# Optimization experiments

Measured on AMD Instinct MI355X. Metric: run time of the kernel, lower is better.

Reference implementation:

```python
import jax, jax.numpy as jnp
import numpy as np

T, B, H = 2048, 8, 1024


def setup_inputs() -> dict:
    key = jax.random.key(0)
    ks = jax.random.split(key, 4)
    scale = 1.0 / np.sqrt(H)
    x = jax.random.normal(ks[0], (T, B, H), dtype=jnp.float32)
    W_q = jax.random.normal(ks[1], (H, H), dtype=jnp.float32) * scale
    b_q = jnp.zeros((H,), dtype=jnp.float32)
    beta_raw = jax.random.normal(ks[2], (H,), dtype=jnp.float32)
    W_fc = jax.random.normal(ks[3], (H, H), dtype=jnp.float32) * scale
    b_fc = jnp.zeros((H,), dtype=jnp.float32)
    return {"x": x, "W_q": W_q, "b_q": b_q, "beta_raw": beta_raw,
            "W_fc": W_fc, "b_fc": b_fc}


def reference(x, W_q, b_q, beta_raw, W_fc, b_fc):
    # Per-neuron learned leak in (0,1)
    beta = jax.nn.sigmoid(beta_raw)  # (H,)
    # Input (q) projection: (T,B,H) @ (H,H)^T
    q = jnp.einsum('tbh,oh->tbo', x, W_q) + b_q  # (T,B,H)
    # Leaky integration m_t = beta * m_{t-1} + q_t as an associative scan over T
    a = jnp.broadcast_to(beta, q.shape)  # (T,B,H)

    def combine(c1, c2):
        a1, m1 = c1
        a2, m2 = c2
        return (a1 * a2, a2 * m1 + m2)

    _, m = jax.lax.associative_scan(combine, (a, q), axis=0)  # (T,B,H)
    # Linear + ReLU
    h = jnp.einsum('tbh,oh->tbo', m, W_fc) + b_fc
    return jax.nn.relu(h)
```

## Files before the change

kernel.cpp:

```cpp
#include <hip/hip_runtime.h>
#include <stdint.h>

typedef unsigned short u16;
typedef __bf16 bf16x8 __attribute__((ext_vector_type(8)));
typedef float f32x4 __attribute__((ext_vector_type(4)));

__device__ __forceinline__ u16 f2bf(float f) {
  union { float f; uint32_t u; } x; x.f = f;
  uint32_t u = x.u;
  u += 0x7fffu + ((u >> 16) & 1u);
  return (u16)(u >> 16);
}
__device__ __forceinline__ float bf2f(uint32_t lo16) {
  union { uint32_t u; float f; } x; x.u = lo16 << 16; return x.f;
}

__device__ __forceinline__ void async_load16(const u16* g, u16* l) {
  __builtin_amdgcn_global_load_lds(
      (const __attribute__((address_space(1))) void*)g,
      (__attribute__((address_space(3))) void*)l,
      16, 0, 0);
}

__global__ __launch_bounds__(256) void prep_all(const float* __restrict__ x,
                                                const float* __restrict__ Wq,
                                                const float* __restrict__ Wfc,
                                                const float* __restrict__ braw,
                                                u16* __restrict__ xb,
                                                u16* __restrict__ wqb,
                                                u16* __restrict__ wfcb,
                                                float* __restrict__ beta) {
  int gid = blockIdx.x * 256 + threadIdx.x;
  if (gid < 1024) beta[gid] = 1.0f / (1.0f + expf(-braw[gid]));
  if (gid < 131072) {
    const int HH = 1024 * 1024;
    int i = gid * 16;
    const float* src = (i < HH) ? (Wq + i) : (Wfc + (i - HH));
    u16* dst = (i < HH) ? (wqb + i) : (wfcb + (i - HH));
#pragma unroll
    for (int c = 0; c < 4; c++) {
      float4 v = *(const float4*)(src + c * 4);
      ushort4 o = {f2bf(v.x), f2bf(v.y), f2bf(v.z), f2bf(v.w)};
      *(ushort4*)(dst + c * 4) = o;
    }
  }
  {
    int i = gid * 8;
    float4 a = *(const float4*)(x + i);
    float4 b = *(const float4*)(x + i + 4);
    ushort4 o0 = {f2bf(a.x), f2bf(a.y), f2bf(a.z), f2bf(a.w)};
    ushort4 o1 = {f2bf(b.x), f2bf(b.y), f2bf(b.z), f2bf(b.w)};
    *(ushort4*)(xb + i) = o0;
    *(ushort4*)(xb + i + 4) = o1;
  }
}

template <int RELU, int OUTBF>
__global__ __launch_bounds__(256) void gemm_bt(const u16* __restrict__ A,
                                               const u16* __restrict__ B,
                                               const float* __restrict__ bias,
                                               void* __restrict__ Cout,
                                               int M, int N, int K) {
  __shared__ u16 As[128 * 64];
  __shared__ u16 Bs[128 * 64];

  const int tid  = threadIdx.x;
  const int lane = tid & 63;

  const int L  = blockIdx.x;
  const int xc = L & 7;
  const int k8 = L >> 3;
  const int tile_n = (k8 & 7) * 128;
  const int tile_m = ((xc << 4) | (k8 >> 3)) * 128;

  const int wm = ((tid >> 7) & 1) * 64;
  const int wn = ((tid >> 6) & 1) * 64;

  const int srow   = tid >> 3;
  const int schunk = (tid & 7) ^ ((tid >> 3) & 7);
  u16* ldsA = &As[((tid >> 6) * 8) * 64];
  u16* ldsB = &Bs[((tid >> 6) * 8) * 64];

  const u16* gA = A + (size_t)(tile_m + srow) * K + schunk * 8;
  const u16* gB = B + (size_t)(tile_n + srow) * K + schunk * 8;

  f32x4 acc[4][4];
#pragma unroll
  for (int i = 0; i < 4; i++)
#pragma unroll
    for (int j = 0; j < 4; j++) acc[i][j] = (f32x4){0.f, 0.f, 0.f, 0.f};

  const int lrow = lane & 15;
  const int kq   = lane >> 4;

  for (int k0 = 0; k0 < K; k0 += 64) {
    __syncthreads();
#pragma unroll
    for (int i = 0; i < 4; i++) {
      async_load16(gA + (size_t)(i * 32) * K + k0, ldsA + i * 32 * 64);
      async_load16(gB + (size_t)(i * 32) * K + k0, ldsB + i * 32 * 64);
    }
    __builtin_amdgcn_s_waitcnt(0);
    __syncthreads();

#pragma unroll
    for (int js = 0; js < 2; js++) {
      const int cc = ((kq + 4 * js) ^ (lane & 7)) << 3;
      bf16x8 a[4], b[4];
#pragma unroll
      for (int i = 0; i < 4; i++)
        a[i] = *(const bf16x8*)&As[(wm + i * 16 + lrow) * 64 + cc];
#pragma unroll
      for (int j = 0; j < 4; j++)
        b[j] = *(const bf16x8*)&Bs[(wn + j * 16 + lrow) * 64 + cc];
#pragma unroll
      for (int i = 0; i < 4; i++)
#pragma unroll
        for (int j = 0; j < 4; j++)
          acc[i][j] = __builtin_amdgcn_mfma_f32_16x16x32_bf16(a[i], b[j], acc[i][j], 0, 0, 0);
    }
  }

  const int crow = (lane >> 4) << 2;
  const int ccol = lane & 15;
#pragma unroll
  for (int i = 0; i < 4; i++) {
#pragma unroll
    for (int j = 0; j < 4; j++) {
      const int gm = tile_m + wm + i * 16 + crow;
      const int gn = tile_n + wn + j * 16 + ccol;
      const float bv = bias[gn];
#pragma unroll
      for (int r = 0; r < 4; r++) {
        float v = acc[i][j][r] + bv;
        if (RELU) v = fmaxf(v, 0.f);
        if (OUTBF) ((u16*)Cout)[(size_t)(gm + r) * N + gn] = f2bf(v);
        else       ((float*)Cout)[(size_t)(gm + r) * N + gn] = v;
      }
    }
  }
}

#define NCH 8192
#define SEG 32
#define NSEG 64

__global__ __launch_bounds__(256) void scan_carry(const uint2* __restrict__ qb,
                                                  float* __restrict__ carry,
                                                  const float* __restrict__ beta_arr) {
  int tid = blockIdx.x * 256 + threadIdx.x;
  int seg = tid >> 11;
  int cq  = tid & 2047;
  int h0  = (cq * 4) & 1023;
  float b0 = beta_arr[h0], b1 = beta_arr[h0 + 1], b2 = beta_arr[h0 + 2], b3 = beta_arr[h0 + 3];
  const uint2* p = qb + (size_t)seg * SEG * 2048 + cq;
  float m0 = 0.f, m1 = 0.f, m2 = 0.f, m3 = 0.f;
#pragma unroll 8
  for (int t = 0; t < SEG; t++) {
    uint2 v = p[(size_t)t * 2048];
    m0 = fmaf(b0, m0, bf2f(v.x & 0xffffu));
    m1 = fmaf(b1, m1, bf2f(v.x >> 16));
    m2 = fmaf(b2, m2, bf2f(v.y & 0xffffu));
    m3 = fmaf(b3, m3, bf2f(v.y >> 16));
  }
  *(float4*)&carry[(size_t)seg * NCH + cq * 4] = make_float4(m0, m1, m2, m3);
}

__global__ __launch_bounds__(256) void scan_fuse(const uint2* __restrict__ qb,
                                                 const float4* __restrict__ carry4,
                                                 const float* __restrict__ beta_arr,
                                                 uint2* __restrict__ mb) {
  const int tid = blockIdx.x * 256 + threadIdx.x;
  const int seg = tid >> 11;
  const int cq  = tid & 2047;
  const int h0  = (cq * 4) & 1023;
  const float b0 = beta_arr[h0], b1 = beta_arr[h0 + 1];
  const float b2 = beta_arr[h0 + 2], b3 = beta_arr[h0 + 3];
  float s0 = b0, s1 = b1, s2 = b2, s3 = b3;
#pragma unroll
  for (int i = 0; i < 5; i++) { s0 *= s0; s1 *= s1; s2 *= s2; s3 *= s3; }
  float m0 = 0.f, m1 = 0.f, m2 = 0.f, m3 = 0.f;
  const float4* cp = carry4 + cq;
  for (int s = 0; s < seg; s++) {
    float4 c = cp[(size_t)s * 2048];
    m0 = fmaf(s0, m0, c.x); m1 = fmaf(s1, m1, c.y);
    m2 = fmaf(s2, m2, c.z); m3 = fmaf(s3, m3, c.w);
  }
  const uint2* p = qb + (size_t)seg * SEG * 2048 + cq;
  uint2* o = mb + (size_t)seg * SEG * 2048 + cq;
#pragma unroll 8
  for (int t = 0; t < SEG; t++) {
    uint2 v = p[(size_t)t * 2048];
    m0 = fmaf(b0, m0, bf2f(v.x & 0xffffu));
    m1 = fmaf(b1, m1, bf2f(v.x >> 16));
    m2 = fmaf(b2, m2, bf2f(v.y & 0xffffu));
    m3 = fmaf(b3, m3, bf2f(v.y >> 16));
    uint2 w;
    w.x = (uint32_t)f2bf(m0) | ((uint32_t)f2bf(m1) << 16);
    w.y = (uint32_t)f2bf(m2) | ((uint32_t)f2bf(m3) << 16);
    o[(size_t)t * 2048] = w;
  }
}

extern "C" void kernel_launch(void* const* d_in, const int* in_sizes, int n_in,
                              void* d_out, int out_size, void* d_ws, size_t ws_size,
                              hipStream_t stream) {
  const float* x        = (const float*)d_in[0];
  const float* W_q      = (const float*)d_in[1];
  const float* b_q      = (const float*)d_in[2];
  const float* beta_raw = (const float*)d_in[3];
  const float* W_fc     = (const float*)d_in[4];
  const float* b_fc     = (const float*)d_in[5];

  const int H = 1024;
  const int M = 2048 * 8;
  const size_t MH = (size_t)M * H;

  char* ws = (char*)d_ws;
  u16* x_bf    = (u16*)ws;  ws += MH * 2;
  u16* q_bf    = (u16*)ws;  ws += MH * 2;
  u16* m_bf    = (u16*)ws;  ws += MH * 2;
  u16* wq_bf   = (u16*)ws;  ws += (size_t)H * H * 2;
  u16* wfc_bf  = (u16*)ws;  ws += (size_t)H * H * 2;
  float* beta  = (float*)ws; ws += 4096;
  float* carry = (float*)ws; ws += (size_t)NSEG * NCH * 4;

  prep_all<<<(int)(MH / 8 / 256), 256, 0, stream>>>(x, W_q, W_fc, beta_raw,
                                                    x_bf, wq_bf, wfc_bf, beta);

  gemm_bt<0, 1><<<1024, 256, 0, stream>>>(x_bf, wq_bf, b_q, q_bf, M, H, H);

  scan_carry<<<NSEG * (NCH / 4) / 256, 256, 0, stream>>>((const uint2*)q_bf, carry, beta);
  scan_fuse<<<NSEG * (NCH / 4) / 256, 256, 0, stream>>>((const uint2*)q_bf,
                                                        (const float4*)carry, beta,
                                                        (uint2*)m_bf);

  gemm_bt<1, 0><<<1024, 256, 0, stream>>>(m_bf, wfc_bf, b_fc, d_out, M, H, H);
}
```

Before: 251.9 us.

## Fuse two-pass scan into single kernel with flag-based inter-block carry propagation

Result: slower. 316.4 us (+25.6%).

```diff
diff --git a/kernel.cpp b/kernel.cpp
--- a/kernel.cpp
+++ b/kernel.cpp
@@ -29,8 +29,10 @@
                                                 u16* __restrict__ xb,
                                                 u16* __restrict__ wqb,
                                                 u16* __restrict__ wfcb,
-                                                float* __restrict__ beta) {
+                                                float* __restrict__ beta,
+                                                uint32_t* __restrict__ flags) {
   int gid = blockIdx.x * 256 + threadIdx.x;
+  if (gid < 512) flags[gid] = 0;
   if (gid < 1024) beta[gid] = 1.0f / (1.0f + expf(-braw[gid]));
   if (gid < 131072) {
     const int HH = 1024 * 1024;
@@ -141,60 +143,70 @@
   }
 }
 
-#define NCH 8192
 #define SEG 32
 #define NSEG 64
 
-__global__ __launch_bounds__(256) void scan_carry(const uint2* __restrict__ qb,
-                                                  float* __restrict__ carry,
-                                                  const float* __restrict__ beta_arr) {
-  int tid = blockIdx.x * 256 + threadIdx.x;
-  int seg = tid >> 11;
-  int cq  = tid & 2047;
-  int h0  = (cq * 4) & 1023;
-  float b0 = beta_arr[h0], b1 = beta_arr[h0 + 1], b2 = beta_arr[h0 + 2], b3 = beta_arr[h0 + 3];
-  const uint2* p = qb + (size_t)seg * SEG * 2048 + cq;
-  float m0 = 0.f, m1 = 0.f, m2 = 0.f, m3 = 0.f;
-#pragma unroll 8
-  for (int t = 0; t < SEG; t++) {
-    uint2 v = p[(size_t)t * 2048];
-    m0 = fmaf(b0, m0, bf2f(v.x & 0xffffu));
-    m1 = fmaf(b1, m1, bf2f(v.x >> 16));
-    m2 = fmaf(b2, m2, bf2f(v.y & 0xffffu));
-    m3 = fmaf(b3, m3, bf2f(v.y >> 16));
-  }
-  *(float4*)&carry[(size_t)seg * NCH + cq * 4] = make_float4(m0, m1, m2, m3);
-}
-
-__global__ __launch_bounds__(256) void scan_fuse(const uint2* __restrict__ qb,
-                                                 const float4* __restrict__ carry4,
-                                                 const float* __restrict__ beta_arr,
-                                                 uint2* __restrict__ mb) {
-  const int tid = blockIdx.x * 256 + threadIdx.x;
-  const int seg = tid >> 11;
-  const int cq  = tid & 2047;
+__global__ __launch_bounds__(256) void scan_one(const uint2* __restrict__ qb,
+                                                float* __restrict__ carry,
+                                                uint32_t* __restrict__ flags,
+                                                const float* __restrict__ beta_arr,
+                                                uint2* __restrict__ mb) {
+  const int seg = blockIdx.x >> 3;
+  const int g   = blockIdx.x & 7;
+  const int cq  = g * 256 + threadIdx.x;
   const int h0  = (cq * 4) & 1023;
   const float b0 = beta_arr[h0], b1 = beta_arr[h0 + 1];
   const float b2 = beta_arr[h0 + 2], b3 = beta_arr[h0 + 3];
+
+  uint2 qr[SEG];
+  const uint2* p = qb + (size_t)seg * SEG * 2048 + cq;
+#pragma unroll
+  for (int t = 0; t < SEG; t++) qr[t] = p[(size_t)t * 2048];
+
+  float c0 = 0.f, c1 = 0.f, c2 = 0.f, c3 = 0.f;
+#pragma unroll
+  for (int t = 0; t < SEG; t++) {
+    c0 = fmaf(b0, c0, bf2f(qr[t].x & 0xffffu));
+    c1 = fmaf(b1, c1, bf2f(qr[t].x >> 16));
+    c2 = fmaf(b2, c2, bf2f(qr[t].y & 0xffffu));
+    c3 = fmaf(b3, c3, bf2f(qr[t].y >> 16));
+  }
+
+  {
+    float* cw = carry + (size_t)seg * 8192 + (size_t)cq * 4;
+    *(float4*)cw = make_float4(c0, c1, c2, c3);
+  }
+  __threadfence();
+  __syncthreads();
+  if (threadIdx.x == 0) atomicExch(&flags[blockIdx.x], 1u);
+
+  if ((int)threadIdx.x < seg) {
+    while (__hip_atomic_load(&flags[threadIdx.x * 8 + g],
+                             __ATOMIC_ACQUIRE, __HIP_MEMORY_SCOPE_AGENT) == 0) {}
+  }
+  __syncthreads();
+
   float s0 = b0, s1 = b1, s2 = b2, s3 = b3;
 #pragma unroll
   for (int i = 0; i < 5; i++) { s0 *= s0; s1 *= s1; s2 *= s2; s3 *= s3; }
   float m0 = 0.f, m1 = 0.f, m2 = 0.f, m3 = 0.f;
-  const float4* cp = carry4 + cq;
-  for (int s = 0; s < seg; s++) {
-    float4 c = cp[(size_t)s * 2048];
-    m0 = fmaf(s0, m0, c.x); m1 = fmaf(s1, m1, c.y);
-    m2 = fmaf(s2, m2, c.z); m3 = fmaf(s3, m3, c.w);
-  }
-  const uint2* p = qb + (size_t)seg * SEG * 2048 + cq;
+  for (int j = 0; j < seg; j++) {
+    const float* cr = carry + (size_t)j * 8192 + (size_t)cq * 4;
+    float v0 = __hip_atomic_load(cr + 0, __ATOMIC_RELAXED, __HIP_MEMORY_SCOPE_AGENT);
+    float v1 = __hip_atomic_load(cr + 1, __ATOMIC_RELAXED, __HIP_MEMORY_SCOPE_AGENT);
+    float v2 = __hip_atomic_load(cr + 2, __ATOMIC_RELAXED, __HIP_MEMORY_SCOPE_AGENT);
+    float v3 = __hip_atomic_load(cr + 3, __ATOMIC_RELAXED, __HIP_MEMORY_SCOPE_AGENT);
+    m0 = fmaf(s0, m0, v0); m1 = fmaf(s1, m1, v1);
+    m2 = fmaf(s2, m2, v2); m3 = fmaf(s3, m3, v3);
+  }
+
   uint2* o = mb + (size_t)seg * SEG * 2048 + cq;
-#pragma unroll 8
+#pragma unroll
   for (int t = 0; t < SEG; t++) {
-    uint2 v = p[(size_t)t * 2048];
-    m0 = fmaf(b0, m0, bf2f(v.x & 0xffffu));
-    m1 = fmaf(b1, m1, bf2f(v.x >> 16));
-    m2 = fmaf(b2, m2, bf2f(v.y & 0xffffu));
-    m3 = fmaf(b3, m3, bf2f(v.y >> 16));
+    m0 = fmaf(b0, m0, bf2f(qr[t].x & 0xffffu));
+    m1 = fmaf(b1, m1, bf2f(qr[t].x >> 16));
+    m2 = fmaf(b2, m2, bf2f(qr[t].y & 0xffffu));
+    m3 = fmaf(b3, m3, bf2f(qr[t].y >> 16));
     uint2 w;
     w.x = (uint32_t)f2bf(m0) | ((uint32_t)f2bf(m1) << 16);
     w.y = (uint32_t)f2bf(m2) | ((uint32_t)f2bf(m3) << 16);
@@ -223,17 +235,16 @@
   u16* wq_bf   = (u16*)ws;  ws += (size_t)H * H * 2;
   u16* wfc_bf  = (u16*)ws;  ws += (size_t)H * H * 2;
   float* beta  = (float*)ws; ws += 4096;
-  float* carry = (float*)ws; ws += (size_t)NSEG * NCH * 4;
+  float* carry = (float*)ws; ws += (size_t)NSEG * 8192 * 4;
+  uint32_t* flags = (uint32_t*)ws; ws += 4096;
 
   prep_all<<<(int)(MH / 8 / 256), 256, 0, stream>>>(x, W_q, W_fc, beta_raw,
-                                                    x_bf, wq_bf, wfc_bf, beta);
+                                                    x_bf, wq_bf, wfc_bf, beta, flags);
 
   gemm_bt<0, 1><<<1024, 256, 0, stream>>>(x_bf, wq_bf, b_q, q_bf, M, H, H);
 
-  scan_carry<<<NSEG * (NCH / 4) / 256, 256, 0, stream>>>((const uint2*)q_bf, carry, beta);
-  scan_fuse<<<NSEG * (NCH / 4) / 256, 256, 0, stream>>>((const uint2*)q_bf,
-                                                        (const float4*)carry, beta,
-                                                        (uint2*)m_bf);
+  scan_one<<<512, 256, 0, stream>>>((const uint2*)q_bf, carry, flags, beta,
+                                    (uint2*)m_bf);
 
   gemm_bt<1, 0><<<1024, 256, 0, stream>>>(m_bf, wfc_bf, b_fc, d_out, M, H, H);
 }
```
